# Kernel tuning notes

Hardware: AMD Instinct MI355X
Metric: run time of the kernel (lower is better)

Reference implementation:

```python
import jax, jax.numpy as jnp
import numpy as np

N = 100000
E = 3200000
IN_DIM = 3
HID = 256
OUT_DIM = 3


def setup_inputs() -> dict:
    key = jax.random.key(0)
    ks = jax.random.split(key, 12)
    x = jax.random.normal(ks[0], (N, IN_DIM), dtype=jnp.float32)
    edge_index = jax.random.randint(ks[1], (2, E), 0, N, dtype=jnp.int64)
    def lin(k, fi, fo):
        k1, k2 = jax.random.split(k)
        bound = 1.0 / np.sqrt(fi)
        W = jax.random.uniform(k1, (fi, fo), jnp.float32, -bound, bound)
        b = jax.random.uniform(k2, (fo,), jnp.float32, -bound, bound)
        return W, b
    W0, b0 = lin(ks[2], IN_DIM, HID)
    W1, b1 = lin(ks[3], HID, HID)
    W2, b2 = lin(ks[4], HID, HID)
    W3, b3 = lin(ks[5], HID, OUT_DIM)
    Wr, br = lin(ks[6], IN_DIM, OUT_DIM)
    return {"x": x, "edge_index": edge_index,
            "W0": W0, "b0": b0, "W1": W1, "b1": b1,
            "W2": W2, "b2": b2, "W3": W3, "b3": b3,
            "Wr": Wr, "br": br}


def reference(x, edge_index, W0, b0, W1, b1, W2, b2, W3, b3, Wr, br):
    n = x.shape[0]
    # add self loops, mirroring build_adjacency_matrix
    loops = jnp.arange(n, dtype=edge_index.dtype)
    row = jnp.concatenate([edge_index[0], loops])
    col = jnp.concatenate([edge_index[1], loops])
    # degree of row endpoints, D^{-1/2}[row] * D^{-1/2}[col] edge weights
    deg = jax.ops.segment_sum(jnp.ones_like(row, dtype=x.dtype), row, num_segments=n)
    dinv = jnp.where(deg > 0, jax.lax.rsqrt(deg), 0.0)
    norm = dinv[row] * dinv[col]  # [E+N]

    def propagate(h):
        # A_hat @ h : gather source features, scale, scatter-add to rows
        return jax.ops.segment_sum(norm[:, None] * h[col], row, num_segments=n)

    h = jax.nn.relu(propagate(x) @ W0 + b0)
    h = jax.nn.relu(propagate(h) @ W1 + b1)
    h = jax.nn.relu(propagate(h) @ W2 + b2)
    h = propagate(h) @ W3 + b3  # last layer: no relu
    return h + (x @ Wr + br)
```

## Files before the change

### kernel.cpp

```cpp
#include <hip/hip_runtime.h>
#include <stdint.h>

typedef unsigned short u16;
typedef unsigned int u32;
typedef __attribute__((ext_vector_type(8))) short short8;
typedef __attribute__((ext_vector_type(4))) float f32x4;
typedef __attribute__((ext_vector_type(2))) unsigned int u32x2;

#define CAP 6144
#define TILE 4096

__device__ __forceinline__ float b2f_bits(u32 bits){ union{u32 u; float f;} v; v.u=bits; return v.f; }
__device__ __forceinline__ float bf_lo(u32 w){ return b2f_bits(w<<16); }
__device__ __forceinline__ float bf_hi(u32 w){ return b2f_bits(w & 0xffff0000u); }
__device__ __forceinline__ u16 f2bf(float f){
  union{float f; u32 u;} v; v.f=f;
  return (u16)((v.u + 0x7fffu + ((v.u>>16)&1u))>>16);
}


__global__ void detect_k(const long long* __restrict__ ei, int* __restrict__ flag,
                         int* __restrict__ gcur, int n, int E, int nbuck){
  __shared__ int sh[256];
  int t = threadIdx.x;
  for(int i=t; i<nbuck; i+=256) gcur[i]=0;
  int lim = E/2 < 2048 ? E/2 : 2048;
  int bad = 0;
  for(int e=t; e<lim; e+=256){
    unsigned long long v = (unsigned long long)ei[e];
    if(v >= (unsigned long long)n) bad = 1;
  }
  sh[t]=bad; __syncthreads();
  for(int off=128; off>0; off>>=1){ if(t<off) sh[t] |= sh[t+off]; __syncthreads(); }
  if(t==0) *flag = sh[0];
}

__device__ __forceinline__ int edge_at(const void* eiv, int is32, long long idx){
  return is32 ? ((const int*)eiv)[idx] : (int)((const long long*)eiv)[idx];
}
__device__ __forceinline__ int clampi(int v, int lo, int hi){
  return v < lo ? lo : (v > hi ? hi : v);
}

__global__ __launch_bounds__(256) void binA_k(const void* __restrict__ eiv, const int* __restrict__ flag,
                        int* __restrict__ gcur, u32* __restrict__ gbuf, int E, int n, int nbuck){
  __shared__ int hist[1024];
  __shared__ int base[1024];
  __shared__ int cur[1024];
  __shared__ int wsum[256];
  __shared__ u32 stage[TILE];
  int t = threadIdx.x;
  long long e0 = (long long)blockIdx.x * TILE;
  int cnt = (int)((long long)E - e0 < TILE ? (long long)E - e0 : TILE);
  int is32 = *flag;
  for(int i=t; i<nbuck; i+=256){ hist[i]=0; cur[i]=0; }
  __syncthreads();
  int eb[16]; u32 ep[16]; int ec=0;
  #pragma unroll
  for(int k=0;k<16;k++){
    int i = t + k*256;
    if(i<cnt){
      long long e = e0 + i;
      int r = clampi(edge_at(eiv,is32,e),0,n-1);
      int c = clampi(edge_at(eiv,is32,(long long)E+e),0,n-1);
      eb[ec] = r>>7;
      ep[ec] = ((u32)(r&127)<<17) | (u32)c;
      atomicAdd(&hist[eb[ec]],1);
      ec++;
    }
  }
  __syncthreads();
  int l[4]; int tot=0;
  #pragma unroll
  for(int j=0;j<4;j++){ int idx=t*4+j; l[j]=(idx<nbuck)?hist[idx]:0; tot+=l[j]; }
  wsum[t]=tot; __syncthreads();
  for(int off=1;off<256;off<<=1){
    int x = (t>=off)?wsum[t-off]:0;
    __syncthreads();
    wsum[t]+=x;
    __syncthreads();
  }
  int excl = wsum[t]-tot;
  #pragma unroll
  for(int j=0;j<4;j++){ int idx=t*4+j; if(idx<nbuck) base[idx]=excl; excl+=l[j]; }
  __syncthreads();
  for(int k=0;k<ec;k++){
    int b = eb[k];
    int slot = base[b] + atomicAdd(&cur[b],1);
    stage[slot] = ep[k];
  }
  __syncthreads();
  for(int b=t; b<nbuck; b+=256){
    int c = hist[b];
    if(c>0){
      int g = atomicAdd(&gcur[b], c);
      if(g > CAP) g = CAP;
      if(g + c > CAP) c = CAP - g;
      int src = base[b];
      u32* dst = gbuf + (size_t)b*CAP + g;
      for(int k=0;k<c;k++) dst[k] = stage[src+k];
    }
  }
}

__global__ __launch_bounds__(256) void scanG_k(const int* __restrict__ gcnt, int* __restrict__ gstart, int nbuck){
  __shared__ int sh[256];
  int t = threadIdx.x;
  int v[4]; int s=0;
  #pragma unroll
  for(int j=0;j<4;j++){
    int idx=t*4+j;
    int c = (idx<nbuck)?gcnt[idx]:0;
    if(c>CAP) c=CAP;
    v[j]=c; s+=c;
  }
  sh[t]=s; __syncthreads();
  for(int off=1;off<256;off<<=1){
    int x=(t>=off)?sh[t-off]:0;
    __syncthreads();
    sh[t]+=x;
    __syncthreads();
  }
  int excl = sh[t]-s;
  #pragma unroll
  for(int j=0;j<4;j++){ int idx=t*4+j; if(idx<nbuck) gstart[idx]=excl; excl+=v[j]; }
}

__global__ __launch_bounds__(256) void csrB_k(const int* __restrict__ gcnt, const int* __restrict__ gstart,
                        const u32* __restrict__ gbuf, int* __restrict__ deg, float* __restrict__ dinv,
                        int* __restrict__ rs, int* __restrict__ csr, int n, int nbuck){
  __shared__ int h[128], lst[128], lcur[128], sc[128];
  __shared__ int colstage[CAP];
  int b = blockIdx.x, t = threadIdx.x;
  if(t<128){ h[t]=0; lcur[t]=0; }
  __syncthreads();
  int c = gcnt[b]; if(c>CAP) c=CAP;
  const u32* p = gbuf + (size_t)b*CAP;
  for(int i=t;i<c;i+=256) atomicAdd(&h[p[i]>>17],1);
  __syncthreads();
  int dv=0;
  if(t<128){ dv=h[t]; sc[t]=dv; }
  __syncthreads();
  for(int off=1;off<128;off<<=1){
    int x=(t>=off&&t<128)?sc[t-off]:0;
    __syncthreads();
    if(t<128) sc[t]+=x;
    __syncthreads();
  }
  int g0 = gstart[b];
  if(t<128){
    lst[t]=sc[t]-dv;
    int row=b*128+t;
    if(row<n){
      deg[row]=dv;
      dinv[row]=rsqrtf((float)(dv+1));
      rs[row]=g0+lst[t];
    }
  }
  __syncthreads();
  for(int i=t;i<c;i+=256){
    u32 pr=p[i];
    int rl=pr>>17;
    int slot=lst[rl]+atomicAdd(&lcur[rl],1);
    if(slot<CAP) colstage[slot]=(int)(pr&0x1FFFFu);
  }
  __syncthreads();
  for(int i=t;i<c;i+=256) csr[g0+i]=colstage[i];
}

__global__ void pack2_k(const float* __restrict__ W1, const float* __restrict__ W2,
                        u16* __restrict__ o1, u16* __restrict__ o2){
  int bid = blockIdx.x;
  const float* W = (bid<256)? W1 : W2;
  u16* out = (bid<256)? o1 : o2;
  int idx = (bid&255)*256 + threadIdx.x;
  int j  = idx & 7;
  int l  = (idx>>3) & 63;
  int ct = (idx>>9) & 15;
  int kk = idx>>13;
  int k  = kk*32 + (l>>4)*8 + j;
  int nn = ct*16 + (l&15);
  out[idx] = f2bf(W[k*256 + nn]);
}

__global__ __launch_bounds__(256) void gemm0f_k(const float* __restrict__ x, const int* __restrict__ csr,
                        const int* __restrict__ rs, const int* __restrict__ deg,
                        const float* __restrict__ dinv, const float* __restrict__ W0,
                        const float* __restrict__ b0, u16* __restrict__ h1, int n){
  __shared__ float s0[256], s1[256], s2[256];
  __shared__ float pr[3];
  int i = blockIdx.x;
  int t = threadIdx.x;
  int s = rs[i], d = deg[i];
  float a0=0.f, a1=0.f, a2=0.f;
  for(int e=t; e<d; e+=256){
    int c = csr[s+e];
    float w = dinv[c];
    a0 += w*x[c*3+0]; a1 += w*x[c*3+1]; a2 += w*x[c*3+2];
  }
  s0[t]=a0; s1[t]=a1; s2[t]=a2; __syncthreads();
  for(int off=128; off>0; off>>=1){
    if(t<off){ s0[t]+=s0[t+off]; s1[t]+=s1[t+off]; s2[t]+=s2[t+off]; }
    __syncthreads();
  }
  if(t==0){
    float di = dinv[i];
    pr[0] = di*(s0[0] + di*x[i*3+0]);
    pr[1] = di*(s1[0] + di*x[i*3+1]);
    pr[2] = di*(s2[0] + di*x[i*3+2]);
  }
  __syncthreads();
  float v = pr[0]*W0[t] + pr[1]*W0[256+t] + pr[2]*W0[512+t] + b0[t];
  v = fmaxf(v, 0.f) * dinv[i];
  h1[(size_t)i*256 + t] = f2bf(v);
}

__global__ __launch_bounds__(256) void prop256_k(const u16* __restrict__ hin, u16* __restrict__ pout,
                          const int* __restrict__ csr, const int* __restrict__ rs,
                          const int* __restrict__ deg, const float* __restrict__ dinv, int n){
  int row = (blockIdx.x*256 + threadIdx.x) >> 6;
  if(row>=n) return;
  row = __builtin_amdgcn_readfirstlane(row);
  int lane = threadIdx.x & 63;
  int co = lane*4;
  const u16* hb = hin + co;
  uint2 sv = *(const uint2*)(hb + (size_t)row*256);
  float a0=bf_lo(sv.x), a1=bf_hi(sv.x), a2=bf_lo(sv.y), a3=bf_hi(sv.y);
  int s = __builtin_amdgcn_readfirstlane(rs[row]);
  int d = __builtin_amdgcn_readfirstlane(deg[row]);
  for(int base=0; base<d; base+=16){
    int cc[16]; u32 mk[16];
    #pragma unroll
    for(int j=0;j<16;j++){
      int ok = (base+j) < d;
      cc[j] = csr[ok ? (s+base+j) : s];
      mk[j] = ok ? 0xffffffffu : 0u;
    }
    uint2 v[16];
    #pragma unroll
    for(int j=0;j<16;j++) v[j] = *(const uint2*)(hb + (size_t)cc[j]*256);
    #pragma unroll
    for(int j=0;j<16;j++){
      u32 xw = v[j].x & mk[j], yw = v[j].y & mk[j];
      a0 += bf_lo(xw); a1 += bf_hi(xw); a2 += bf_lo(yw); a3 += bf_hi(yw);
    }
  }
  float sc = dinv[row];
  u32x2 o;
  o.x = (u32)f2bf(a0*sc) | ((u32)f2bf(a1*sc)<<16);
  o.y = (u32)f2bf(a2*sc) | ((u32)f2bf(a3*sc)<<16);
  __builtin_nontemporal_store(o, (u32x2*)(pout + (size_t)row*256 + co));
}

__global__ __launch_bounds__(256) void gemm256_k(const u16* __restrict__ A, const u16* __restrict__ Bp,
                          const float* __restrict__ bias, const float* __restrict__ dinv,
                          u16* __restrict__ Out, int M){
  int wave = threadIdx.x>>6, lane = threadIdx.x&63;
  int rowbase = blockIdx.x*64 + wave*16;
  f32x4 acc[16];
  #pragma unroll
  for(int t=0;t<16;t++){ acc[t][0]=0.f; acc[t][1]=0.f; acc[t][2]=0.f; acc[t][3]=0.f; }
  const u16* Ap = A + (size_t)(rowbase + (lane&15))*256 + ((lane>>4)*8);
  const u16* Bl = Bp + (size_t)lane*8;
  #pragma unroll
  for(int kk=0; kk<8; kk++){
    short8 af = __builtin_nontemporal_load((const short8*)(Ap + kk*32));
    const u16* bb = Bl + (size_t)kk*8192;
    #pragma unroll
    for(int t=0;t<16;t++){
      short8 bf = *(const short8*)(bb + t*512);
      acc[t] = __builtin_amdgcn_mfma_f32_16x16x32_bf16(af, bf, acc[t], 0, 0, 0);
    }
  }
  int r0 = rowbase + (lane>>4)*4;
  float dv[4]; bool ok[4];
  #pragma unroll
  for(int r=0;r<4;r++){ ok[r] = (r0+r) < M; dv[r] = ok[r] ? dinv[r0+r] : 0.f; }
  #pragma unroll
  for(int t=0;t<16;t++){
    int col = t*16 + (lane&15);
    float bc = bias[col];
    #pragma unroll
    for(int r=0;r<4;r++){
      if(ok[r]){
        float v = fmaxf(acc[t][r] + bc, 0.f) * dv[r];
        Out[(size_t)(r0+r)*256 + col] = f2bf(v);
      }
    }
  }
}

__global__ __launch_bounds__(256) void gemm256w3_k(const u16* __restrict__ A, const u16* __restrict__ Bp,
                          const float* __restrict__ bias, const float* __restrict__ dinv,
                          const float* __restrict__ W3, float* __restrict__ qh, int M){
  __shared__ float w3s[768];
  for(int i=threadIdx.x; i<768; i+=256) w3s[i] = W3[i];
  __syncthreads();
  int wave = threadIdx.x>>6, lane = threadIdx.x&63;
  int rowbase = blockIdx.x*64 + wave*16;
  f32x4 acc[16];
  #pragma unroll
  for(int t=0;t<16;t++){ acc[t][0]=0.f; acc[t][1]=0.f; acc[t][2]=0.f; acc[t][3]=0.f; }
  const u16* Ap = A + (size_t)(rowbase + (lane&15))*256 + ((lane>>4)*8);
  const u16* Bl = Bp + (size_t)lane*8;
  #pragma unroll
  for(int kk=0; kk<8; kk++){
    short8 af = __builtin_nontemporal_load((const short8*)(Ap + kk*32));
    const u16* bb = Bl + (size_t)kk*8192;
    #pragma unroll
    for(int t=0;t<16;t++){
      short8 bf = *(const short8*)(bb + t*512);
      acc[t] = __builtin_amdgcn_mfma_f32_16x16x32_bf16(af, bf, acc[t], 0, 0, 0);
    }
  }
  int r0 = rowbase + (lane>>4)*4;
  int cl = lane & 15;
  float dv[4];
  #pragma unroll
  for(int r=0;r<4;r++) dv[r] = (r0+r) < M ? dinv[r0+r] : 0.f;
  float q0[4]={0,0,0,0}, q1[4]={0,0,0,0}, q2[4]={0,0,0,0};
  #pragma unroll
  for(int t=0;t<16;t++){
    int col = t*16 + cl;
    float bc = bias[col];
    float w30=w3s[col*3+0], w31=w3s[col*3+1], w32=w3s[col*3+2];
    #pragma unroll
    for(int r=0;r<4;r++){
      float v = fmaxf(acc[t][r] + bc, 0.f) * dv[r];
      q0[r] += v*w30; q1[r] += v*w31; q2[r] += v*w32;
    }
  }
  #pragma unroll
  for(int off=1; off<16; off<<=1){
    #pragma unroll
    for(int r=0;r<4;r++){
      q0[r] += __shfl_xor(q0[r], off);
      q1[r] += __shfl_xor(q1[r], off);
      q2[r] += __shfl_xor(q2[r], off);
    }
  }
  if(cl==0){
    #pragma unroll
    for(int r=0;r<4;r++){
      int row = r0 + r;
      if(row < M){
        qh[row*3+0]=q0[r]; qh[row*3+1]=q1[r]; qh[row*3+2]=q2[r];
      }
    }
  }
}

__global__ __launch_bounds__(256) void final2_k(const float* __restrict__ qh, const float* __restrict__ x,
                        const int* __restrict__ csr, const int* __restrict__ rs,
                        const int* __restrict__ deg, const float* __restrict__ dinv,
                        const float* __restrict__ b3, const float* __restrict__ Wr,
                        const float* __restrict__ br, float* __restrict__ out, int n){
  int row = (blockIdx.x*256 + threadIdx.x) >> 6;
  if(row>=n) return;
  row = __builtin_amdgcn_readfirstlane(row);
  int lane = threadIdx.x & 63;
  int s = __builtin_amdgcn_readfirstlane(rs[row]);
  int d = __builtin_amdgcn_readfirstlane(deg[row]);
  float a0=0.f, a1=0.f, a2=0.f;
  for(int e=lane; e<d; e+=64){
    int c = csr[s+e];
    a0 += qh[c*3+0]; a1 += qh[c*3+1]; a2 += qh[c*3+2];
  }
  #pragma unroll
  for(int off=32; off>0; off>>=1){
    a0 += __shfl_xor(a0, off);
    a1 += __shfl_xor(a1, off);
    a2 += __shfl_xor(a2, off);
  }
  if(lane==0){
    float di = dinv[row];
    a0 = di*(a0 + qh[row*3+0]);
    a1 = di*(a1 + qh[row*3+1]);
    a2 = di*(a2 + qh[row*3+2]);
    float x0=x[row*3+0], x1=x[row*3+1], x2=x[row*3+2];
    out[row*3+0] = a0 + b3[0] + x0*Wr[0] + x1*Wr[3] + x2*Wr[6] + br[0];
    out[row*3+1] = a1 + b3[1] + x0*Wr[1] + x1*Wr[4] + x2*Wr[7] + br[1];
    out[row*3+2] = a2 + b3[2] + x0*Wr[2] + x1*Wr[5] + x2*Wr[8] + br[2];
  }
}

extern "C" void kernel_launch(void* const* d_in, const int* in_sizes, int n_in,
                              void* d_out, int out_size, void* d_ws, size_t ws_size,
                              hipStream_t stream) {
  const float* x  = (const float*)d_in[0];
  const void*  ei = d_in[1];
  const float* W0 = (const float*)d_in[2];
  const float* b0 = (const float*)d_in[3];
  const float* W1 = (const float*)d_in[4];
  const float* b1 = (const float*)d_in[5];
  const float* W2 = (const float*)d_in[6];
  const float* b2 = (const float*)d_in[7];
  const float* W3 = (const float*)d_in[8];
  const float* b3 = (const float*)d_in[9];
  const float* Wr = (const float*)d_in[10];
  const float* br = (const float*)d_in[11];
  float* out = (float*)d_out;

  int n = in_sizes[0]/3;
  int E = in_sizes[1]/2;
  int nbuck = (n+127)>>7;
  int Mpad = ((n+63)/64)*64;

  char* p = (char*)d_ws;
  auto alloc = [&](size_t bytes)->char*{ char* r=p; p += (bytes+255)&~(size_t)255; return r; };
  int*   gcur  = (int*)  alloc((size_t)nbuck*4);
  int*   gstart= (int*)  alloc((size_t)nbuck*4);
  int*   deg   = (int*)  alloc((size_t)n*4);
  float* dinv  = (float*)alloc((size_t)n*4);
  int*   rs    = (int*)  alloc((size_t)n*4);
  int*   flag  = (int*)  alloc(256);
  int*   csr   = (int*)  alloc((size_t)E*4);
  u16*   hA    = (u16*)  alloc((size_t)Mpad*512);
  u16*   hB    = (u16*)  alloc((size_t)Mpad*512);
  float* qh    = (float*)alloc((size_t)n*12);
  u16*   W1p   = (u16*)  alloc(65536*2);
  u16*   W2p   = (u16*)  alloc(65536*2);
  u32*   gbuf  = (u32*)hA;

  int gA  = (E+TILE-1)/TILE;
  int gp  = (n*64+255)/256;

  detect_k<<<1, 256, 0, stream>>>((const long long*)ei, flag, gcur, n, E, nbuck);
  binA_k  <<<gA, 256, 0, stream>>>(ei, flag, gcur, gbuf, E, n, nbuck);
  scanG_k <<<1, 256, 0, stream>>>(gcur, gstart, nbuck);
  csrB_k  <<<nbuck, 256, 0, stream>>>(gcur, gstart, gbuf, deg, dinv, rs, csr, n, nbuck);

  pack2_k <<<512, 256, 0, stream>>>(W1, W2, W1p, W2p);

  gemm0f_k<<<n, 256, 0, stream>>>(x, csr, rs, deg, dinv, W0, b0, hA, n);

  prop256_k<<<gp, 256, 0, stream>>>(hA, hB, csr, rs, deg, dinv, n);
  gemm256_k<<<Mpad/64, 256, 0, stream>>>(hB, W1p, b1, dinv, hA, n);

  prop256_k<<<gp, 256, 0, stream>>>(hA, hB, csr, rs, deg, dinv, n);
  gemm256w3_k<<<Mpad/64, 256, 0, stream>>>(hB, W2p, b2, dinv, W3, qh, n);

  final2_k<<<gp, 256, 0, stream>>>(qh, x, csr, rs, deg, dinv, b3, Wr, br, out, n);
}
```

Before: 875.9 us.

## Use wave-per-row layer-0 kernel and column-sliced propagation with shuffle reduction

The first-layer kernel now handles one row per 64-lane wave instead of one row per 256-thread block. It reduces the neighbour sums with cross-lane shuffles rather than shared memory and barriers, and each lane writes four output columns. The 256-wide propagation kernel is split into eight 32-column slices per group of 16 rows, with 16 lanes per row each gathering one packed bf16 pair. Because the blocks for each slice touch a narrower band of the feature matrix, gathers should reuse L2 cache better. In exchange, each CSR neighbour list is read eight times and each gather moves fewer bytes per request.

```diff
diff --git a/kernel.cpp b/kernel.cpp
--- a/kernel.cpp
+++ b/kernel.cpp
@@ -5,7 +5,6 @@
 typedef unsigned int u32;
 typedef __attribute__((ext_vector_type(8))) short short8;
 typedef __attribute__((ext_vector_type(4))) float f32x4;
-typedef __attribute__((ext_vector_type(2))) unsigned int u32x2;
 
 #define CAP 6144
 #define TILE 4096
@@ -183,73 +182,83 @@
   out[idx] = f2bf(W[k*256 + nn]);
 }
 
-__global__ __launch_bounds__(256) void gemm0f_k(const float* __restrict__ x, const int* __restrict__ csr,
+__global__ __launch_bounds__(256) void gemm0w_k(const float* __restrict__ x, const int* __restrict__ csr,
                         const int* __restrict__ rs, const int* __restrict__ deg,
                         const float* __restrict__ dinv, const float* __restrict__ W0,
                         const float* __restrict__ b0, u16* __restrict__ h1, int n){
-  __shared__ float s0[256], s1[256], s2[256];
-  __shared__ float pr[3];
-  int i = blockIdx.x;
-  int t = threadIdx.x;
-  int s = rs[i], d = deg[i];
+  int i = (blockIdx.x*256 + threadIdx.x) >> 6;
+  if(i>=n) return;
+  i = __builtin_amdgcn_readfirstlane(i);
+  int lane = threadIdx.x & 63;
+  int s = __builtin_amdgcn_readfirstlane(rs[i]);
+  int d = __builtin_amdgcn_readfirstlane(deg[i]);
   float a0=0.f, a1=0.f, a2=0.f;
-  for(int e=t; e<d; e+=256){
+  for(int e=lane; e<d; e+=64){
     int c = csr[s+e];
     float w = dinv[c];
     a0 += w*x[c*3+0]; a1 += w*x[c*3+1]; a2 += w*x[c*3+2];
   }
-  s0[t]=a0; s1[t]=a1; s2[t]=a2; __syncthreads();
-  for(int off=128; off>0; off>>=1){
-    if(t<off){ s0[t]+=s0[t+off]; s1[t]+=s1[t+off]; s2[t]+=s2[t+off]; }
-    __syncthreads();
-  }
-  if(t==0){
-    float di = dinv[i];
-    pr[0] = di*(s0[0] + di*x[i*3+0]);
-    pr[1] = di*(s1[0] + di*x[i*3+1]);
-    pr[2] = di*(s2[0] + di*x[i*3+2]);
-  }
-  __syncthreads();
-  float v = pr[0]*W0[t] + pr[1]*W0[256+t] + pr[2]*W0[512+t] + b0[t];
-  v = fmaxf(v, 0.f) * dinv[i];
-  h1[(size_t)i*256 + t] = f2bf(v);
-}
-
-__global__ __launch_bounds__(256) void prop256_k(const u16* __restrict__ hin, u16* __restrict__ pout,
+  #pragma unroll
+  for(int off=32; off>0; off>>=1){
+    a0 += __shfl_xor(a0, off);
+    a1 += __shfl_xor(a1, off);
+    a2 += __shfl_xor(a2, off);
+  }
+  float di = dinv[i];
+  float p0 = di*(a0 + di*x[i*3+0]);
+  float p1 = di*(a1 + di*x[i*3+1]);
+  float p2 = di*(a2 + di*x[i*3+2]);
+  int c0 = lane*4;
+  float v[4];
+  #pragma unroll
+  for(int j=0;j<4;j++){
+    int col = c0 + j;
+    float t = p0*W0[col] + p1*W0[256+col] + p2*W0[512+col] + b0[col];
+    v[j] = fmaxf(t, 0.f) * di;
+  }
+  uint2 o;
+  o.x = (u32)f2bf(v[0]) | ((u32)f2bf(v[1])<<16);
+  o.y = (u32)f2bf(v[2]) | ((u32)f2bf(v[3])<<16);
+  *(uint2*)(h1 + (size_t)i*256 + c0) = o;
+}
+
+__global__ __launch_bounds__(256) void prop256s_k(const u16* __restrict__ hin, u16* __restrict__ pout,
                           const int* __restrict__ csr, const int* __restrict__ rs,
                           const int* __restrict__ deg, const float* __restrict__ dinv, int n){
-  int row = (blockIdx.x*256 + threadIdx.x) >> 6;
-  if(row>=n) return;
-  row = __builtin_amdgcn_readfirstlane(row);
-  int lane = threadIdx.x & 63;
-  int co = lane*4;
-  const u16* hb = hin + co;
-  uint2 sv = *(const uint2*)(hb + (size_t)row*256);
-  float a0=bf_lo(sv.x), a1=bf_hi(sv.x), a2=bf_lo(sv.y), a3=bf_hi(sv.y);
-  int s = __builtin_amdgcn_readfirstlane(rs[row]);
-  int d = __builtin_amdgcn_readfirstlane(deg[row]);
-  for(int base=0; base<d; base+=16){
-    int cc[16]; u32 mk[16];
-    #pragma unroll
-    for(int j=0;j<16;j++){
+  int b = blockIdx.x;
+  int q = b & 7;
+  int rowg = b >> 3;
+  int t = threadIdx.x;
+  int w = t >> 6, l = t & 63;
+  int g = l >> 4, li = l & 15;
+  int row = rowg*16 + w*4 + g;
+  if(row >= n) return;
+  int col = q*32 + li*2;
+  const u16* hb = hin + col;
+  u32 sv = *(const u32*)(hb + (size_t)row*256);
+  float a0 = bf_lo(sv), a1 = bf_hi(sv);
+  int s = __builtin_nontemporal_load(&rs[row]);
+  int d = __builtin_nontemporal_load(&deg[row]);
+  for(int base=0; base<d; base+=8){
+    int cc[8]; u32 mk[8];
+    #pragma unroll
+    for(int j=0;j<8;j++){
       int ok = (base+j) < d;
-      cc[j] = csr[ok ? (s+base+j) : s];
+      cc[j] = __builtin_nontemporal_load(&csr[ok ? (s+base+j) : s]);
       mk[j] = ok ? 0xffffffffu : 0u;
     }
-    uint2 v[16];
-    #pragma unroll
-    for(int j=0;j<16;j++) v[j] = *(const uint2*)(hb + (size_t)cc[j]*256);
-    #pragma unroll
-    for(int j=0;j<16;j++){
-      u32 xw = v[j].x & mk[j], yw = v[j].y & mk[j];
-      a0 += bf_lo(xw); a1 += bf_hi(xw); a2 += bf_lo(yw); a3 += bf_hi(yw);
+    u32 v[8];
+    #pragma unroll
+    for(int j=0;j<8;j++) v[j] = *(const u32*)(hb + (size_t)cc[j]*256);
+    #pragma unroll
+    for(int j=0;j<8;j++){
+      u32 xw = v[j] & mk[j];
+      a0 += bf_lo(xw); a1 += bf_hi(xw);
     }
   }
   float sc = dinv[row];
-  u32x2 o;
-  o.x = (u32)f2bf(a0*sc) | ((u32)f2bf(a1*sc)<<16);
-  o.y = (u32)f2bf(a2*sc) | ((u32)f2bf(a3*sc)<<16);
-  __builtin_nontemporal_store(o, (u32x2*)(pout + (size_t)row*256 + co));
+  u32 o = (u32)f2bf(a0*sc) | ((u32)f2bf(a1*sc)<<16);
+  __builtin_nontemporal_store(o, (u32*)(pout + (size_t)row*256 + col));
 }
 
 __global__ __launch_bounds__(256) void gemm256_k(const u16* __restrict__ A, const u16* __restrict__ Bp,
@@ -424,6 +433,7 @@
 
   int gA  = (E+TILE-1)/TILE;
   int gp  = (n*64+255)/256;
+  int gps = ((n+15)/16) * 8;
 
   detect_k<<<1, 256, 0, stream>>>((const long long*)ei, flag, gcur, n, E, nbuck);
   binA_k  <<<gA, 256, 0, stream>>>(ei, flag, gcur, gbuf, E, n, nbuck);
@@ -432,12 +442,12 @@
 
   pack2_k <<<512, 256, 0, stream>>>(W1, W2, W1p, W2p);
 
-  gemm0f_k<<<n, 256, 0, stream>>>(x, csr, rs, deg, dinv, W0, b0, hA, n);
-
-  prop256_k<<<gp, 256, 0, stream>>>(hA, hB, csr, rs, deg, dinv, n);
+  gemm0w_k<<<gp, 256, 0, stream>>>(x, csr, rs, deg, dinv, W0, b0, hA, n);
+
+  prop256s_k<<<gps, 256, 0, stream>>>(hA, hB, csr, rs, deg, dinv, n);
   gemm256_k<<<Mpad/64, 256, 0, stream>>>(hB, W1p, b1, dinv, hA, n);
 
-  prop256_k<<<gp, 256, 0, stream>>>(hA, hB, csr, rs, deg, dinv, n);
+  prop256s_k<<<gps, 256, 0, stream>>>(hA, hB, csr, rs, deg, dinv, n);
   gemm256w3_k<<<Mpad/64, 256, 0, stream>>>(hB, W2p, b2, dinv, W3, qh, n);
 
   final2_k<<<gp, 256, 0, stream>>>(qh, x, csr, rs, deg, dinv, b3, Wr, br, out, n);
```

After: 1.348 ms. 53.9% more time.

## Fuse setup kernels and remap first-layer aggregation to one wavefront per node

Applied to the files above, without the earlier changes.

Removes the separate detect, scan and weight-pack kernels by folding index-width detection into the binning kernel, the bucket prefix scan into each CSR-build block, and weight packing into the first-layer kernel. The first-layer aggregation switches from one 256-thread block per node with shared-memory reduction to one wavefront per node with shuffle reductions and vectorized bf16 stores. This cuts launch overhead and idle threads, at the cost of redundant per-block detection and scan work.

```diff
diff --git a/kernel.cpp b/kernel.cpp
--- a/kernel.cpp
+++ b/kernel.cpp
@@ -18,23 +18,6 @@
   return (u16)((v.u + 0x7fffu + ((v.u>>16)&1u))>>16);
 }
 
-
-__global__ void detect_k(const long long* __restrict__ ei, int* __restrict__ flag,
-                         int* __restrict__ gcur, int n, int E, int nbuck){
-  __shared__ int sh[256];
-  int t = threadIdx.x;
-  for(int i=t; i<nbuck; i+=256) gcur[i]=0;
-  int lim = E/2 < 2048 ? E/2 : 2048;
-  int bad = 0;
-  for(int e=t; e<lim; e+=256){
-    unsigned long long v = (unsigned long long)ei[e];
-    if(v >= (unsigned long long)n) bad = 1;
-  }
-  sh[t]=bad; __syncthreads();
-  for(int off=128; off>0; off>>=1){ if(t<off) sh[t] |= sh[t+off]; __syncthreads(); }
-  if(t==0) *flag = sh[0];
-}
-
 __device__ __forceinline__ int edge_at(const void* eiv, int is32, long long idx){
   return is32 ? ((const int*)eiv)[idx] : (int)((const long long*)eiv)[idx];
 }
@@ -42,7 +25,8 @@
   return v < lo ? lo : (v > hi ? hi : v);
 }
 
-__global__ __launch_bounds__(256) void binA_k(const void* __restrict__ eiv, const int* __restrict__ flag,
+
+__global__ __launch_bounds__(256) void binA_k(const void* __restrict__ eiv,
                         int* __restrict__ gcur, u32* __restrict__ gbuf, int E, int n, int nbuck){
   __shared__ int hist[1024];
   __shared__ int base[1024];
@@ -50,9 +34,20 @@
   __shared__ int wsum[256];
   __shared__ u32 stage[TILE];
   int t = threadIdx.x;
+  {
+    int lim = E/2 < 2048 ? E/2 : 2048;
+    int bad = 0;
+    const long long* e64 = (const long long*)eiv;
+    for(int e=t; e<lim; e+=256){
+      if((unsigned long long)e64[e] >= (unsigned long long)n) bad = 1;
+    }
+    wsum[t]=bad; __syncthreads();
+    for(int off=128; off>0; off>>=1){ if(t<off) wsum[t] |= wsum[t+off]; __syncthreads(); }
+  }
+  int is32 = wsum[0];
+  __syncthreads();
   long long e0 = (long long)blockIdx.x * TILE;
   int cnt = (int)((long long)E - e0 < TILE ? (long long)E - e0 : TILE);
-  int is32 = *flag;
   for(int i=t; i<nbuck; i+=256){ hist[i]=0; cur[i]=0; }
   __syncthreads();
   int eb[16]; u32 ep[16]; int ec=0;
@@ -103,9 +98,14 @@
   }
 }
 
-__global__ __launch_bounds__(256) void scanG_k(const int* __restrict__ gcnt, int* __restrict__ gstart, int nbuck){
-  __shared__ int sh[256];
-  int t = threadIdx.x;
+__global__ __launch_bounds__(256) void csrB_k(const int* __restrict__ gcnt,
+                        const u32* __restrict__ gbuf, int* __restrict__ deg, float* __restrict__ dinv,
+                        int* __restrict__ rs, int* __restrict__ csr, int n, int nbuck){
+  __shared__ int gsc[1024];
+  __shared__ int wsum[256];
+  __shared__ int h[128], lst[128], lcur[128], sc[128];
+  __shared__ int colstage[CAP];
+  int b = blockIdx.x, t = threadIdx.x;
   int v[4]; int s=0;
   #pragma unroll
   for(int j=0;j<4;j++){
@@ -114,26 +114,19 @@
     if(c>CAP) c=CAP;
     v[j]=c; s+=c;
   }
-  sh[t]=s; __syncthreads();
+  wsum[t]=s; __syncthreads();
   for(int off=1;off<256;off<<=1){
-    int x=(t>=off)?sh[t-off]:0;
-    __syncthreads();
-    sh[t]+=x;
-    __syncthreads();
-  }
-  int excl = sh[t]-s;
-  #pragma unroll
-  for(int j=0;j<4;j++){ int idx=t*4+j; if(idx<nbuck) gstart[idx]=excl; excl+=v[j]; }
-}
-
-__global__ __launch_bounds__(256) void csrB_k(const int* __restrict__ gcnt, const int* __restrict__ gstart,
-                        const u32* __restrict__ gbuf, int* __restrict__ deg, float* __restrict__ dinv,
-                        int* __restrict__ rs, int* __restrict__ csr, int n, int nbuck){
-  __shared__ int h[128], lst[128], lcur[128], sc[128];
-  __shared__ int colstage[CAP];
-  int b = blockIdx.x, t = threadIdx.x;
+    int x=(t>=off)?wsum[t-off]:0;
+    __syncthreads();
+    wsum[t]+=x;
+    __syncthreads();
+  }
+  int excl = wsum[t]-s;
+  #pragma unroll
+  for(int j=0;j<4;j++){ int idx=t*4+j; if(idx<nbuck) gsc[idx]=excl; excl+=v[j]; }
   if(t<128){ h[t]=0; lcur[t]=0; }
   __syncthreads();
+  int g0 = gsc[b];
   int c = gcnt[b]; if(c>CAP) c=CAP;
   const u32* p = gbuf + (size_t)b*CAP;
   for(int i=t;i<c;i+=256) atomicAdd(&h[p[i]>>17],1);
@@ -147,7 +140,6 @@
     if(t<128) sc[t]+=x;
     __syncthreads();
   }
-  int g0 = gstart[b];
   if(t<128){
     lst[t]=sc[t]-dv;
     int row=b*128+t;
@@ -168,51 +160,59 @@
   for(int i=t;i<c;i+=256) csr[g0+i]=colstage[i];
 }
 
-__global__ void pack2_k(const float* __restrict__ W1, const float* __restrict__ W2,
-                        u16* __restrict__ o1, u16* __restrict__ o2){
-  int bid = blockIdx.x;
-  const float* W = (bid<256)? W1 : W2;
-  u16* out = (bid<256)? o1 : o2;
-  int idx = (bid&255)*256 + threadIdx.x;
-  int j  = idx & 7;
-  int l  = (idx>>3) & 63;
-  int ct = (idx>>9) & 15;
-  int kk = idx>>13;
-  int k  = kk*32 + (l>>4)*8 + j;
-  int nn = ct*16 + (l&15);
-  out[idx] = f2bf(W[k*256 + nn]);
-}
-
-__global__ __launch_bounds__(256) void gemm0f_k(const float* __restrict__ x, const int* __restrict__ csr,
+__global__ __launch_bounds__(256) void gemm0w_k(const float* __restrict__ x, const int* __restrict__ csr,
                         const int* __restrict__ rs, const int* __restrict__ deg,
                         const float* __restrict__ dinv, const float* __restrict__ W0,
-                        const float* __restrict__ b0, u16* __restrict__ h1, int n){
-  __shared__ float s0[256], s1[256], s2[256];
-  __shared__ float pr[3];
-  int i = blockIdx.x;
-  int t = threadIdx.x;
-  int s = rs[i], d = deg[i];
+                        const float* __restrict__ b0, u16* __restrict__ h1,
+                        const float* __restrict__ W1, const float* __restrict__ W2,
+                        u16* __restrict__ W1p, u16* __restrict__ W2p, int n){
+  if(blockIdx.x < 512){
+    int bid = blockIdx.x;
+    const float* W = (bid<256)? W1 : W2;
+    u16* o = (bid<256)? W1p : W2p;
+    int idx = (bid&255)*256 + threadIdx.x;
+    int j  = idx & 7;
+    int l  = (idx>>3) & 63;
+    int ct = (idx>>9) & 15;
+    int kk = idx>>13;
+    int k  = kk*32 + (l>>4)*8 + j;
+    int nn = ct*16 + (l&15);
+    o[idx] = f2bf(W[k*256 + nn]);
+  }
+  int i = (blockIdx.x*256 + threadIdx.x) >> 6;
+  if(i>=n) return;
+  i = __builtin_amdgcn_readfirstlane(i);
+  int lane = threadIdx.x & 63;
+  int s = __builtin_amdgcn_readfirstlane(rs[i]);
+  int d = __builtin_amdgcn_readfirstlane(deg[i]);
   float a0=0.f, a1=0.f, a2=0.f;
-  for(int e=t; e<d; e+=256){
+  for(int e=lane; e<d; e+=64){
     int c = csr[s+e];
     float w = dinv[c];
     a0 += w*x[c*3+0]; a1 += w*x[c*3+1]; a2 += w*x[c*3+2];
   }
-  s0[t]=a0; s1[t]=a1; s2[t]=a2; __syncthreads();
-  for(int off=128; off>0; off>>=1){
-    if(t<off){ s0[t]+=s0[t+off]; s1[t]+=s1[t+off]; s2[t]+=s2[t+off]; }
-    __syncthreads();
-  }
-  if(t==0){
-    float di = dinv[i];
-    pr[0] = di*(s0[0] + di*x[i*3+0]);
-    pr[1] = di*(s1[0] + di*x[i*3+1]);
-    pr[2] = di*(s2[0] + di*x[i*3+2]);
-  }
-  __syncthreads();
-  float v = pr[0]*W0[t] + pr[1]*W0[256+t] + pr[2]*W0[512+t] + b0[t];
-  v = fmaxf(v, 0.f) * dinv[i];
-  h1[(size_t)i*256 + t] = f2bf(v);
+  #pragma unroll
+  for(int off=32; off>0; off>>=1){
+    a0 += __shfl_xor(a0, off);
+    a1 += __shfl_xor(a1, off);
+    a2 += __shfl_xor(a2, off);
+  }
+  float di = dinv[i];
+  float p0 = di*(a0 + di*x[i*3+0]);
+  float p1 = di*(a1 + di*x[i*3+1]);
+  float p2 = di*(a2 + di*x[i*3+2]);
+  int c0 = lane*4;
+  float v[4];
+  #pragma unroll
+  for(int j=0;j<4;j++){
+    int col = c0 + j;
+    float t = p0*W0[col] + p1*W0[256+col] + p2*W0[512+col] + b0[col];
+    v[j] = fmaxf(t, 0.f) * di;
+  }
+  uint2 o;
+  o.x = (u32)f2bf(v[0]) | ((u32)f2bf(v[1])<<16);
+  o.y = (u32)f2bf(v[2]) | ((u32)f2bf(v[3])<<16);
+  *(uint2*)(h1 + (size_t)i*256 + c0) = o;
 }
 
 __global__ __launch_bounds__(256) void prop256_k(const u16* __restrict__ hin, u16* __restrict__ pout,
@@ -409,11 +409,9 @@
   char* p = (char*)d_ws;
   auto alloc = [&](size_t bytes)->char*{ char* r=p; p += (bytes+255)&~(size_t)255; return r; };
   int*   gcur  = (int*)  alloc((size_t)nbuck*4);
-  int*   gstart= (int*)  alloc((size_t)nbuck*4);
   int*   deg   = (int*)  alloc((size_t)n*4);
   float* dinv  = (float*)alloc((size_t)n*4);
   int*   rs    = (int*)  alloc((size_t)n*4);
-  int*   flag  = (int*)  alloc(256);
   int*   csr   = (int*)  alloc((size_t)E*4);
   u16*   hA    = (u16*)  alloc((size_t)Mpad*512);
   u16*   hB    = (u16*)  alloc((size_t)Mpad*512);
@@ -425,14 +423,11 @@
   int gA  = (E+TILE-1)/TILE;
   int gp  = (n*64+255)/256;
 
-  detect_k<<<1, 256, 0, stream>>>((const long long*)ei, flag, gcur, n, E, nbuck);
-  binA_k  <<<gA, 256, 0, stream>>>(ei, flag, gcur, gbuf, E, n, nbuck);
-  scanG_k <<<1, 256, 0, stream>>>(gcur, gstart, nbuck);
-  csrB_k  <<<nbuck, 256, 0, stream>>>(gcur, gstart, gbuf, deg, dinv, rs, csr, n, nbuck);
-
-  pack2_k <<<512, 256, 0, stream>>>(W1, W2, W1p, W2p);
-
-  gemm0f_k<<<n, 256, 0, stream>>>(x, csr, rs, deg, dinv, W0, b0, hA, n);
+  hipMemsetAsync(gcur, 0, (size_t)nbuck*4, stream);
+  binA_k  <<<gA, 256, 0, stream>>>(ei, gcur, gbuf, E, n, nbuck);
+  csrB_k  <<<nbuck, 256, 0, stream>>>(gcur, gbuf, deg, dinv, rs, csr, n, nbuck);
+
+  gemm0w_k<<<gp, 256, 0, stream>>>(x, csr, rs, deg, dinv, W0, b0, hA, W1, W2, W1p, W2p, n);
 
   prop256_k<<<gp, 256, 0, stream>>>(hA, hB, csr, rs, deg, dinv, n);
   gemm256_k<<<Mpad/64, 256, 0, stream>>>(hB, W1p, b1, dinv, hA, n);
```

Result: faster. 797.2 us (median of 2 runs) (-9.0%).
